# Performance work log

Hardware: AMD Instinct MI355X
Metric: run time of the kernel (lower is better)

The kernel has to match this reference:

```python
import jax, jax.numpy as jnp
import numpy as np

NUM_NODES_GLOBAL = 100000
EMBED_DIM = 256
NUM_RELATIONS = 16
N_LOCAL = 16384
N_EDGES = 131072
N_QUERIES = 4096


def setup_inputs() -> dict:
    key = jax.random.key(0)
    ks = jax.random.split(key, 12)
    node_emb = jax.random.normal(ks[0], (NUM_NODES_GLOBAL, EMBED_DIM), dtype=jnp.float32)
    # RGCN layer 1 params: per-relation weight (R, in, out), root weight, bias
    w1 = jax.random.normal(ks[1], (NUM_RELATIONS, EMBED_DIM, EMBED_DIM), dtype=jnp.float32) * 0.05
    root1 = jax.random.normal(ks[2], (EMBED_DIM, EMBED_DIM), dtype=jnp.float32) * 0.05
    b1 = jnp.zeros((EMBED_DIM,), dtype=jnp.float32)
    w2 = jax.random.normal(ks[3], (NUM_RELATIONS, EMBED_DIM, EMBED_DIM), dtype=jnp.float32) * 0.05
    root2 = jax.random.normal(ks[4], (EMBED_DIM, EMBED_DIM), dtype=jnp.float32) * 0.05
    b2 = jnp.zeros((EMBED_DIM,), dtype=jnp.float32)
    edge_index = jax.random.randint(ks[5], (2, N_EDGES), 0, N_LOCAL, dtype=jnp.int64)
    edge_type = jax.random.randint(ks[6], (N_EDGES,), 0, NUM_RELATIONS, dtype=jnp.int64)
    entity_ids = jax.random.randint(ks[7], (N_LOCAL,), 0, NUM_NODES_GLOBAL, dtype=jnp.int64)
    batch_ids = jnp.sort(jax.random.randint(ks[8], (N_LOCAL,), 0, N_QUERIES, dtype=jnp.int64))
    return {"node_emb": node_emb, "w1": w1, "root1": root1, "b1": b1,
            "w2": w2, "root2": root2, "b2": b2,
            "edge_index": edge_index, "edge_type": edge_type,
            "entity_ids": entity_ids, "batch_ids": batch_ids}


def rgcn_layer(x, W, Wroot, b, src, tgt, edge_type, num_relations):
    """PyG RGCNConv (num_bases=None, aggr='mean', root_weight=True, bias=True).

    out[i] = sum_r mean_{j: (j -r-> i)} x_j @ W[r]  +  x_i @ Wroot + b
    Aggregation done per (target, relation) bucket, then a single (N,R,d)x(R,d,d) einsum.
    """
    n = x.shape[0]
    d = x.shape[1]
    bucket = tgt * num_relations + edge_type  # (E,) combined (node, relation) key
    ones = jnp.ones(src.shape, dtype=x.dtype)
    cnt = jax.ops.segment_sum(ones, bucket, num_segments=n * num_relations)
    agg = jax.ops.segment_sum(x[src], bucket, num_segments=n * num_relations)
    agg = agg.reshape(n, num_relations, d) / jnp.maximum(cnt, 1.0).reshape(n, num_relations, 1)
    return jnp.einsum('nrd,rdo->no', agg, W) + x @ Wroot + b


def reference(node_emb, w1, root1, b1, w2, root2, b2, edge_index, edge_type, entity_ids, batch_ids):
    x = node_emb[entity_ids]                      # (N_local, d) gather from global table
    src, tgt = edge_index[0], edge_index[1]
    x = rgcn_layer(x, w1, root1, b1, src, tgt, edge_type, NUM_RELATIONS)
    x = rgcn_layer(x, w2, root2, b2, src, tgt, edge_type, NUM_RELATIONS)
    # scatter-sum readout per query
    return jax.ops.segment_sum(x, batch_ids, num_segments=N_QUERIES)
```

## Files before the change

kernel.cpp:

```cpp
#include <hip/hip_runtime.h>
#include <hip/hip_bf16.h>

#define NLOCAL 16384
#define NEDGES 131072
#define NREL   16
#define DIM    256
#define NQ     4096
#define NBLKS  512
#define NSLOTS (NEDGES + NREL * 64)
#define NBLKE  (NSLOTS / 64)

typedef __bf16 bf16x8 __attribute__((ext_vector_type(8)));
typedef float  f32x4  __attribute__((ext_vector_type(4)));
typedef unsigned short u16x4 __attribute__((ext_vector_type(4)));
typedef unsigned short u16x8 __attribute__((ext_vector_type(8)));

static __device__ __forceinline__ unsigned short f2bf(float f) {
    union { float f; unsigned u; } v; v.f = f;
    unsigned r = v.u + 0x7FFFu + ((v.u >> 16) & 1u);
    return (unsigned short)(r >> 16);
}
static __device__ __forceinline__ float bf2f(unsigned short s) {
    union { unsigned u; float f; } v; v.u = ((unsigned)s) << 16;
    return v.f;
}

__global__ void k_gather(const float* __restrict__ emb, const int* __restrict__ ids,
                         unsigned short* __restrict__ x0) {
    int gid = blockIdx.x * blockDim.x + threadIdx.x;
    int i = gid >> 5, c8 = gid & 31;
    int e = ids[i];
    const f32x4* src = (const f32x4*)(emb + (size_t)e * DIM + c8 * 8);
    f32x4 a = src[0], b = src[1];
    u16x8 u;
    u[0] = f2bf(a[0]); u[1] = f2bf(a[1]); u[2] = f2bf(a[2]); u[3] = f2bf(a[3]);
    u[4] = f2bf(b[0]); u[5] = f2bf(b[1]); u[6] = f2bf(b[2]); u[7] = f2bf(b[3]);
    *(u16x8*)&x0[(size_t)i * DIM + c8 * 8] = u;
}

__global__ void k_transpose_all(const float* __restrict__ w1, const float* __restrict__ r1,
                                const float* __restrict__ w2, const float* __restrict__ r2,
                                unsigned short* __restrict__ WT1, unsigned short* __restrict__ rT1,
                                unsigned short* __restrict__ WT2, unsigned short* __restrict__ rT2) {
    __shared__ float t[64][65];
    int blk = blockIdx.x;
    const float* W; unsigned short* WT; int tr;
    if (blk < 256)      { W = w1 + (size_t)(blk >> 4) * DIM * DIM; WT = WT1 + (size_t)(blk >> 4) * DIM * DIM; tr = blk & 15; }
    else if (blk < 272) { W = r1; WT = rT1; tr = blk - 256; }
    else if (blk < 528) { int q = blk - 272; W = w2 + (size_t)(q >> 4) * DIM * DIM; WT = WT2 + (size_t)(q >> 4) * DIM * DIM; tr = q & 15; }
    else                { W = r2; WT = rT2; tr = blk - 528; }
    int tk = (tr >> 2) << 6;
    int to = (tr & 3) << 6;
    #pragma unroll
    for (int it = 0; it < 16; ++it) {
        int el = it * 256 + threadIdx.x;
        int row = el >> 6, col = el & 63;
        t[row][col] = W[(size_t)(tk + row) * DIM + to + col];
    }
    __syncthreads();
    #pragma unroll
    for (int it = 0; it < 16; ++it) {
        int el = it * 256 + threadIdx.x;
        int row = el >> 6, col = el & 63;
        WT[(size_t)(to + row) * DIM + tk + col] = f2bf(t[col][row]);
    }
}

__global__ void k_hist2(const int* __restrict__ eidx, const int* __restrict__ etype,
                        unsigned int* __restrict__ cnt, unsigned int* __restrict__ cnt_t,
                        int* __restrict__ bh) {
    __shared__ int h[NREL];
    int tid = threadIdx.x;
    if (tid < NREL) h[tid] = 0;
    __syncthreads();
    int e = blockIdx.x * 256 + tid;
    int rel = etype[e];
    int tgt = eidx[NEDGES + e];
    atomicAdd(&cnt[tgt * NREL + rel], 1u);
    atomicAdd(&cnt_t[tgt], 1u);
    atomicAdd(&h[rel], 1);
    __syncthreads();
    if (tid < NREL) bh[tid * NBLKS + blockIdx.x] = h[tid];
}

__global__ void k_scan_all(int* __restrict__ bh, int* __restrict__ meta,
                           const unsigned int* __restrict__ cnt_t, int* __restrict__ row_ptr,
                           int* __restrict__ cur_t, int* __restrict__ blk_rel) {
    __shared__ int tot[NREL];
    __shared__ int rs[NREL + 1];
    __shared__ int wsum[16];
    int tid = threadIdx.x;
    int w = tid >> 6, lane = tid & 63;

    int vals[8];
    int run = 0;
    #pragma unroll
    for (int c = 0; c < 8; ++c) {
        int v = bh[w * NBLKS + c * 64 + lane];
        int s = v;
        #pragma unroll
        for (int off = 1; off < 64; off <<= 1) {
            int t = __shfl_up(s, off);
            if (lane >= off) s += t;
        }
        vals[c] = run + s - v;
        run += __shfl(s, 63);
    }
    if (lane == 0) tot[w] = run;
    __syncthreads();
    if (tid == 0) {
        int s = 0;
        for (int r = 0; r < NREL; ++r) { rs[r] = s; meta[16 + r] = s; s += (tot[r] + 63) & ~63; }
        rs[NREL] = s; meta[32] = s;
    }
    __syncthreads();
    int b0 = rs[w];
    #pragma unroll
    for (int c = 0; c < 8; ++c) bh[w * NBLKS + c * 64 + lane] = vals[c] + b0;

    int total = rs[NREL];
    for (int b = tid; b < NBLKE; b += 1024) {
        int base = b * 64;
        int r;
        if (base >= total) r = -1;
        else { r = 0; while (r < 15 && rs[r + 1] <= base) ++r; }
        blk_rel[b] = r;
    }

    int base16 = tid * 16;
    int loc[16];
    int s = 0;
    #pragma unroll
    for (int c = 0; c < 16; ++c) { loc[c] = s; s += (int)cnt_t[base16 + c]; }
    int inc = s;
    #pragma unroll
    for (int off = 1; off < 64; off <<= 1) {
        int t = __shfl_up(inc, off);
        if (lane >= off) inc += t;
    }
    if (lane == 63) wsum[w] = inc;
    __syncthreads();
    if (tid == 0) {
        int a = 0;
        for (int q = 0; q < 16; ++q) { int v = wsum[q]; wsum[q] = a; a += v; }
    }
    __syncthreads();
    int excl = wsum[w] + inc - s;
    #pragma unroll
    for (int c = 0; c < 16; ++c) { int v = excl + loc[c]; row_ptr[base16 + c] = v; cur_t[base16 + c] = v; }
    if (tid == 1023) row_ptr[NLOCAL] = excl + s;
}

__global__ void k_place2(const int* __restrict__ eidx, const int* __restrict__ etype,
                         const int* __restrict__ bh, int* __restrict__ ssrc,
                         int* __restrict__ stgt, int* __restrict__ cur_t,
                         int* __restrict__ elist) {
    __shared__ int cur[NREL];
    int tid = threadIdx.x;
    if (tid < NREL) cur[tid] = bh[tid * NBLKS + blockIdx.x];
    __syncthreads();
    int e = blockIdx.x * 256 + tid;
    int rel = etype[e];
    int tgt = eidx[NEDGES + e];
    int pos = atomicAdd(&cur[rel], 1);
    ssrc[pos] = eidx[e];
    stgt[pos] = tgt;
    int q = atomicAdd(&cur_t[tgt], 1);
    elist[q] = pos;
}

#define AS_IDX(row, c16) ((row) * 64 + (((c16) ^ ((row) & 7)) << 3))

__launch_bounds__(256)
__global__ void k_gemm_root(const unsigned short* __restrict__ X, const unsigned short* __restrict__ BT,
                            const float* __restrict__ bias, unsigned short* __restrict__ Y) {
    __shared__ __align__(16) unsigned short smem[16384];
    unsigned short* As0 = smem;
    unsigned short* As1 = smem + 4096;
    int tid = threadIdx.x;
    int wave = tid >> 6, lane = tid & 63;
    int l16 = lane & 15, grp = lane >> 4;
    int bm = blockIdx.x;
    int arow = tid >> 3, ac16 = tid & 7;

    f32x4 acc[4][4];
    #pragma unroll
    for (int i = 0; i < 4; ++i)
        #pragma unroll
        for (int j = 0; j < 4; ++j) acc[i][j] = f32x4{0.f, 0.f, 0.f, 0.f};

    #pragma unroll
    for (int it = 0; it < 2; ++it) {
        int row = it * 32 + arow;
        u16x8 u = *(const u16x8*)&X[(size_t)(bm * 64 + row) * DIM + ac16 * 8];
        *(u16x8*)&As0[AS_IDX(row, ac16)] = u;
    }
    for (int kt = 0; kt < 4; ++kt) {
        __syncthreads();
        if (kt < 3) {
            unsigned short* dst = (kt & 1) ? As0 : As1;
            #pragma unroll
            for (int it = 0; it < 2; ++it) {
                int row = it * 32 + arow;
                u16x8 u = *(const u16x8*)&X[(size_t)(bm * 64 + row) * DIM + (kt + 1) * 64 + ac16 * 8];
                *(u16x8*)&dst[AS_IDX(row, ac16)] = u;
            }
        }
        const unsigned short* buf = (kt & 1) ? As1 : As0;
        bf16x8 b[2][4];
        #pragma unroll
        for (int kk = 0; kk < 2; ++kk)
            #pragma unroll
            for (int j = 0; j < 4; ++j)
                b[kk][j] = *(const bf16x8*)&BT[(size_t)(wave * 64 + j * 16 + l16) * DIM + kt * 64 + kk * 32 + grp * 8];
        #pragma unroll
        for (int kk = 0; kk < 2; ++kk) {
            bf16x8 a[4];
            #pragma unroll
            for (int i = 0; i < 4; ++i)
                a[i] = *(const bf16x8*)&buf[AS_IDX(i * 16 + l16, kk * 4 + grp)];
            #pragma unroll
            for (int i = 0; i < 4; ++i)
                #pragma unroll
                for (int j = 0; j < 4; ++j)
                    acc[i][j] = __builtin_amdgcn_mfma_f32_16x16x32_bf16(a[i], b[kk][j], acc[i][j], 0, 0, 0);
        }
    }
    __syncthreads();
    #pragma unroll
    for (int i = 0; i < 4; ++i)
        #pragma unroll
        for (int reg = 0; reg < 4; ++reg) {
            int row = i * 16 + grp * 4 + reg;
            #pragma unroll
            for (int j = 0; j < 4; ++j) {
                int col = wave * 64 + j * 16 + l16;
                float v = acc[i][j][reg] + bias[col];
                float vo = __shfl_xor(v, 1);
                if (!(lane & 1)) {
                    unsigned pk = (unsigned)f2bf(v) | ((unsigned)f2bf(vo) << 16);
                    *(unsigned*)&smem[row * 256 + col] = pk;
                }
            }
        }
    __syncthreads();
    int r = tid >> 2;
    size_t orow = (size_t)(bm * 64 + r) * DIM;
    #pragma unroll
    for (int it = 0; it < 8; ++it) {
        int ch = (tid & 3) + it * 4;
        *(u16x8*)&Y[orow + ch * 8] = *(const u16x8*)&smem[r * 256 + ch * 8];
    }
}

__launch_bounds__(256)
__global__ void k_gemm_edge(const unsigned short* __restrict__ X, const unsigned short* __restrict__ WT,
                            const int* __restrict__ ssrc, const int* __restrict__ stgt,
                            const unsigned int* __restrict__ cnt, const int* __restrict__ blk_rel,
                            unsigned short* __restrict__ ye) {
    int rel = blk_rel[blockIdx.x];
    if (rel < 0) return;
    int base = blockIdx.x * 64;
    const unsigned short* BT = WT + (size_t)rel * DIM * DIM;

    __shared__ __align__(16) unsigned short smem[16384];
    unsigned short* As0 = smem;
    unsigned short* As1 = smem + 4096;
    int tid = threadIdx.x;
    int wave = tid >> 6, lane = tid & 63;
    int l16 = lane & 15, grp = lane >> 4;
    int arow = tid >> 3, ac16 = tid & 7;

    f32x4 acc[4][4];
    #pragma unroll
    for (int i = 0; i < 4; ++i)
        #pragma unroll
        for (int j = 0; j < 4; ++j) acc[i][j] = f32x4{0.f, 0.f, 0.f, 0.f};

    int s0 = ssrc[base + arow];
    int s1 = ssrc[base + 32 + arow];
    #pragma unroll
    for (int it = 0; it < 2; ++it) {
        int row = it * 32 + arow;
        int s = it ? s1 : s0;
        u16x8 u = {};
        if (s >= 0) u = *(const u16x8*)&X[(size_t)s * DIM + ac16 * 8];
        *(u16x8*)&As0[AS_IDX(row, ac16)] = u;
    }
    for (int kt = 0; kt < 4; ++kt) {
        __syncthreads();
        if (kt < 3) {
            unsigned short* dst = (kt & 1) ? As0 : As1;
            #pragma unroll
            for (int it = 0; it < 2; ++it) {
                int row = it * 32 + arow;
                int s = it ? s1 : s0;
                u16x8 u = {};
                if (s >= 0) u = *(const u16x8*)&X[(size_t)s * DIM + (kt + 1) * 64 + ac16 * 8];
                *(u16x8*)&dst[AS_IDX(row, ac16)] = u;
            }
        }
        const unsigned short* buf = (kt & 1) ? As1 : As0;
        bf16x8 b[2][4];
        #pragma unroll
        for (int kk = 0; kk < 2; ++kk)
            #pragma unroll
            for (int j = 0; j < 4; ++j)
                b[kk][j] = *(const bf16x8*)&BT[(size_t)(wave * 64 + j * 16 + l16) * DIM + kt * 64 + kk * 32 + grp * 8];
        #pragma unroll
        for (int kk = 0; kk < 2; ++kk) {
            bf16x8 a[4];
            #pragma unroll
            for (int i = 0; i < 4; ++i)
                a[i] = *(const bf16x8*)&buf[AS_IDX(i * 16 + l16, kk * 4 + grp)];
            #pragma unroll
            for (int i = 0; i < 4; ++i)
                #pragma unroll
                for (int j = 0; j < 4; ++j)
                    acc[i][j] = __builtin_amdgcn_mfma_f32_16x16x32_bf16(a[i], b[kk][j], acc[i][j], 0, 0, 0);
        }
    }
    __syncthreads();
    #pragma unroll
    for (int i = 0; i < 4; ++i)
        #pragma unroll
        for (int reg = 0; reg < 4; ++reg) {
            int row = i * 16 + grp * 4 + reg;
            int e = base + row;
            int s = ssrc[e];
            int tgt = stgt[e];
            float rc = (s >= 0) ? 1.0f / fmaxf((float)cnt[tgt * NREL + rel], 1.0f) : 0.0f;
            #pragma unroll
            for (int j = 0; j < 4; ++j) {
                int col = wave * 64 + j * 16 + l16;
                float v = acc[i][j][reg] * rc;
                float vo = __shfl_xor(v, 1);
                if (!(lane & 1)) {
                    unsigned pk = (unsigned)f2bf(v) | ((unsigned)f2bf(vo) << 16);
                    *(unsigned*)&smem[row * 256 + col] = pk;
                }
            }
        }
    __syncthreads();
    int r = tid >> 2;
    if (ssrc[base + r] >= 0) {
        size_t orow = (size_t)(base + r) * DIM;
        #pragma unroll
        for (int it = 0; it < 8; ++it) {
            int ch = (tid & 3) + it * 4;
            *(u16x8*)&ye[orow + ch * 8] = *(const u16x8*)&smem[r * 256 + ch * 8];
        }
    }
}

__global__ void k_combine(const unsigned short* __restrict__ rootY, const unsigned short* __restrict__ ye,
                          const int* __restrict__ row_ptr, const int* __restrict__ elist,
                          unsigned short* __restrict__ Xout) {
    int wave = threadIdx.x >> 6, lane = threadIdx.x & 63;
    int tgt = blockIdx.x * 4 + wave;
    int c0 = lane * 4;
    u16x4 rv = *(const u16x4*)&rootY[(size_t)tgt * DIM + c0];
    float a0 = bf2f(rv[0]), a1 = bf2f(rv[1]), a2 = bf2f(rv[2]), a3 = bf2f(rv[3]);
    int p0 = row_ptr[tgt], p1 = row_ptr[tgt + 1];
    for (int p = p0; p < p1; ++p) {
        int idx = elist[p];
        u16x4 v = *(const u16x4*)&ye[(size_t)idx * DIM + c0];
        a0 += bf2f(v[0]); a1 += bf2f(v[1]); a2 += bf2f(v[2]); a3 += bf2f(v[3]);
    }
    u16x4 o;
    o[0] = f2bf(a0); o[1] = f2bf(a1); o[2] = f2bf(a2); o[3] = f2bf(a3);
    *(u16x4*)&Xout[(size_t)tgt * DIM + c0] = o;
}

__global__ void k_readout(const unsigned short* __restrict__ X2, const int* __restrict__ bids,
                          float* __restrict__ out) {
    int gid = blockIdx.x * blockDim.x + threadIdx.x;
    int g = gid >> 5, c8 = gid & 31;
    int i0 = g * 8;
    float a[8];
    #pragma unroll
    for (int j = 0; j < 8; ++j) a[j] = 0.f;
    int curq = bids[i0];
    #pragma unroll
    for (int t = 0; t < 8; ++t) {
        int i = i0 + t;
        int q = bids[i];
        if (q != curq) {
            #pragma unroll
            for (int j = 0; j < 8; ++j) {
                unsafeAtomicAdd(&out[(size_t)curq * DIM + c8 * 8 + j], a[j]);
                a[j] = 0.f;
            }
            curq = q;
        }
        u16x8 v = *(const u16x8*)&X2[(size_t)i * DIM + c8 * 8];
        #pragma unroll
        for (int j = 0; j < 8; ++j) a[j] += bf2f(v[j]);
    }
    #pragma unroll
    for (int j = 0; j < 8; ++j)
        unsafeAtomicAdd(&out[(size_t)curq * DIM + c8 * 8 + j], a[j]);
}

extern "C" void kernel_launch(void* const* d_in, const int* in_sizes, int n_in,
                              void* d_out, int out_size, void* d_ws, size_t ws_size,
                              hipStream_t stream) {
    const float* emb   = (const float*)d_in[0];
    const float* w1    = (const float*)d_in[1];
    const float* root1 = (const float*)d_in[2];
    const float* b1    = (const float*)d_in[3];
    const float* w2    = (const float*)d_in[4];
    const float* root2 = (const float*)d_in[5];
    const float* b2    = (const float*)d_in[6];
    const int* eidx    = (const int*)d_in[7];
    const int* etype   = (const int*)d_in[8];
    const int* eids    = (const int*)d_in[9];
    const int* bids    = (const int*)d_in[10];
    float* out = (float*)d_out;

    char* ws = (char*)d_ws;
    unsigned short* x0   = (unsigned short*)(ws + (size_t)(0 << 20));
    unsigned short* x1   = (unsigned short*)(ws + (size_t)(8 << 20));
    unsigned short* x2   = (unsigned short*)(ws + (size_t)(16 << 20));
    unsigned short* WT1  = (unsigned short*)(ws + (size_t)(24 << 20));
    unsigned short* rT1  = (unsigned short*)(ws + (size_t)(26 << 20));
    unsigned short* WT2  = (unsigned short*)(ws + (size_t)(27 << 20));
    unsigned short* rT2  = (unsigned short*)(ws + (size_t)(29 << 20));
    unsigned int*   cnt  = (unsigned int*)(ws + (size_t)(30 << 20));
    int*           meta  = (int*)(ws + (size_t)(31 << 20));
    int*           ssrc  = (int*)(ws + (size_t)(31 << 20) + 4096);
    int*           stgt  = (int*)(ws + (size_t)(32 << 20));
    int*           bh    = (int*)(ws + (size_t)(33 << 20));
    unsigned int*  cnt_t = (unsigned int*)(ws + (size_t)(33 << 20) + 65536);
    int*         row_ptr = (int*)(ws + (size_t)(33 << 20) + 2 * 65536);
    int*           cur_t = (int*)(ws + (size_t)(33 << 20) + 4 * 65536);
    int*         blk_rel = (int*)(ws + (size_t)(33 << 20) + 6 * 65536);
    int*           elist = (int*)(ws + (size_t)(34 << 20));
    unsigned short* rootY= (unsigned short*)(ws + (size_t)(35 << 20));
    unsigned short* ye   = (unsigned short*)(ws + (size_t)(43 << 20));

    hipMemsetAsync(cnt, 0, (size_t)NLOCAL * NREL * 4, stream);
    hipMemsetAsync(cnt_t, 0, (size_t)NLOCAL * 4, stream);
    hipMemsetAsync(ssrc, 0xFF, (size_t)NSLOTS * 4, stream);
    hipMemsetAsync(out, 0, (size_t)NQ * DIM * 4, stream);

    k_gather<<<2048, 256, 0, stream>>>(emb, eids, x0);
    k_transpose_all<<<544, 256, 0, stream>>>(w1, root1, w2, root2, WT1, rT1, WT2, rT2);
    k_hist2<<<NBLKS, 256, 0, stream>>>(eidx, etype, cnt, cnt_t, bh);
    k_scan_all<<<1, 1024, 0, stream>>>(bh, meta, cnt_t, row_ptr, cur_t, blk_rel);
    k_place2<<<NBLKS, 256, 0, stream>>>(eidx, etype, bh, ssrc, stgt, cur_t, elist);

    k_gemm_root<<<NLOCAL / 64, 256, 0, stream>>>(x0, rT1, b1, rootY);
    k_gemm_edge<<<NBLKE, 256, 0, stream>>>(x0, WT1, ssrc, stgt, cnt, blk_rel, ye);
    k_combine<<<NLOCAL / 4, 256, 0, stream>>>(rootY, ye, row_ptr, elist, x1);
    k_gemm_root<<<NLOCAL / 64, 256, 0, stream>>>(x1, rT2, b2, rootY);
    k_gemm_edge<<<NBLKE, 256, 0, stream>>>(x1, WT2, ssrc, stgt, cnt, blk_rel, ye);
    k_combine<<<NLOCAL / 4, 256, 0, stream>>>(rootY, ye, row_ptr, elist, x2);

    k_readout<<<256, 256, 0, stream>>>(x2, bids, out);
}
```

Before: 468.0 us.

## Use direct global-to-LDS loads in GEMMs and fuse final combine into readout

Both GEMM kernels now fill the A tile with global_load_lds, moving the XOR swizzle to the global address side, and write results straight to global memory instead of staging through LDS. The last layer's combine step is merged into the per-query readout, so the x2 intermediate is no longer written and re-read and one launch is dropped. The trade-offs are narrower, less coalesced output stores and a fused readout whose per-thread edge loops run on only 256 blocks.

New measurement: 465.8 us. No clear change (-0.5%).

```diff
diff --git a/kernel.cpp b/kernel.cpp
--- a/kernel.cpp
+++ b/kernel.cpp
@@ -14,6 +14,9 @@
 typedef float  f32x4  __attribute__((ext_vector_type(4)));
 typedef unsigned short u16x4 __attribute__((ext_vector_type(4)));
 typedef unsigned short u16x8 __attribute__((ext_vector_type(8)));
+
+typedef __attribute__((address_space(1))) const void cglobal_t;
+typedef __attribute__((address_space(3))) void clds_t;
 
 static __device__ __forceinline__ unsigned short f2bf(float f) {
     union { float f; unsigned u; } v; v.f = f;
@@ -174,14 +177,18 @@
 __launch_bounds__(256)
 __global__ void k_gemm_root(const unsigned short* __restrict__ X, const unsigned short* __restrict__ BT,
                             const float* __restrict__ bias, unsigned short* __restrict__ Y) {
-    __shared__ __align__(16) unsigned short smem[16384];
-    unsigned short* As0 = smem;
-    unsigned short* As1 = smem + 4096;
+    __shared__ __align__(16) unsigned short As[2][4096];
     int tid = threadIdx.x;
     int wave = tid >> 6, lane = tid & 63;
     int l16 = lane & 15, grp = lane >> 4;
     int bm = blockIdx.x;
-    int arow = tid >> 3, ac16 = tid & 7;
+
+    int slot0 = (wave * 2 + 0) * 64 + lane;
+    int slot1 = (wave * 2 + 1) * 64 + lane;
+    int row0 = slot0 >> 3, cp0 = slot0 & 7;
+    int row1 = slot1 >> 3, cp1 = slot1 & 7;
+    size_t ga0 = (size_t)(bm * 64 + row0) * DIM + ((cp0 ^ (row0 & 7)) * 8);
+    size_t ga1 = (size_t)(bm * 64 + row1) * DIM + ((cp1 ^ (row1 & 7)) * 8);
 
     f32x4 acc[4][4];
     #pragma unroll
@@ -189,24 +196,17 @@
         #pragma unroll
         for (int j = 0; j < 4; ++j) acc[i][j] = f32x4{0.f, 0.f, 0.f, 0.f};
 
-    #pragma unroll
-    for (int it = 0; it < 2; ++it) {
-        int row = it * 32 + arow;
-        u16x8 u = *(const u16x8*)&X[(size_t)(bm * 64 + row) * DIM + ac16 * 8];
-        *(u16x8*)&As0[AS_IDX(row, ac16)] = u;
-    }
+    __builtin_amdgcn_global_load_lds((cglobal_t*)(X + ga0), (clds_t*)&As[0][slot0 * 8], 16, 0, 0);
+    __builtin_amdgcn_global_load_lds((cglobal_t*)(X + ga1), (clds_t*)&As[0][slot1 * 8], 16, 0, 0);
+
     for (int kt = 0; kt < 4; ++kt) {
         __syncthreads();
         if (kt < 3) {
-            unsigned short* dst = (kt & 1) ? As0 : As1;
-            #pragma unroll
-            for (int it = 0; it < 2; ++it) {
-                int row = it * 32 + arow;
-                u16x8 u = *(const u16x8*)&X[(size_t)(bm * 64 + row) * DIM + (kt + 1) * 64 + ac16 * 8];
-                *(u16x8*)&dst[AS_IDX(row, ac16)] = u;
-            }
-        }
-        const unsigned short* buf = (kt & 1) ? As1 : As0;
+            int nb = (kt + 1) & 1;
+            __builtin_amdgcn_global_load_lds((cglobal_t*)(X + ga0 + (kt + 1) * 64), (clds_t*)&As[nb][slot0 * 8], 16, 0, 0);
+            __builtin_amdgcn_global_load_lds((cglobal_t*)(X + ga1 + (kt + 1) * 64), (clds_t*)&As[nb][slot1 * 8], 16, 0, 0);
+        }
+        const unsigned short* buf = As[kt & 1];
         bf16x8 b[2][4];
         #pragma unroll
         for (int kk = 0; kk < 2; ++kk)
@@ -226,12 +226,12 @@
                     acc[i][j] = __builtin_amdgcn_mfma_f32_16x16x32_bf16(a[i], b[kk][j], acc[i][j], 0, 0, 0);
         }
     }
-    __syncthreads();
     #pragma unroll
     for (int i = 0; i < 4; ++i)
         #pragma unroll
         for (int reg = 0; reg < 4; ++reg) {
             int row = i * 16 + grp * 4 + reg;
+            int gr = bm * 64 + row;
             #pragma unroll
             for (int j = 0; j < 4; ++j) {
                 int col = wave * 64 + j * 16 + l16;
@@ -239,18 +239,10 @@
                 float vo = __shfl_xor(v, 1);
                 if (!(lane & 1)) {
                     unsigned pk = (unsigned)f2bf(v) | ((unsigned)f2bf(vo) << 16);
-                    *(unsigned*)&smem[row * 256 + col] = pk;
+                    *(unsigned*)&Y[(size_t)gr * DIM + col] = pk;
                 }
             }
         }
-    __syncthreads();
-    int r = tid >> 2;
-    size_t orow = (size_t)(bm * 64 + r) * DIM;
-    #pragma unroll
-    for (int it = 0; it < 8; ++it) {
-        int ch = (tid & 3) + it * 4;
-        *(u16x8*)&Y[orow + ch * 8] = *(const u16x8*)&smem[r * 256 + ch * 8];
-    }
 }
 
 __launch_bounds__(256)
@@ -263,13 +255,19 @@
     int base = blockIdx.x * 64;
     const unsigned short* BT = WT + (size_t)rel * DIM * DIM;
 
-    __shared__ __align__(16) unsigned short smem[16384];
-    unsigned short* As0 = smem;
-    unsigned short* As1 = smem + 4096;
+    __shared__ __align__(16) unsigned short As[2][4096];
     int tid = threadIdx.x;
     int wave = tid >> 6, lane = tid & 63;
     int l16 = lane & 15, grp = lane >> 4;
-    int arow = tid >> 3, ac16 = tid & 7;
+
+    int slot0 = (wave * 2 + 0) * 64 + lane;
+    int slot1 = (wave * 2 + 1) * 64 + lane;
+    int row0 = slot0 >> 3, cp0 = slot0 & 7;
+    int row1 = slot1 >> 3, cp1 = slot1 & 7;
+    int s0 = ssrc[base + row0];
+    int s1 = ssrc[base + row1];
+    size_t ga0 = (size_t)(s0 < 0 ? 0 : s0) * DIM + ((cp0 ^ (row0 & 7)) * 8);
+    size_t ga1 = (size_t)(s1 < 0 ? 0 : s1) * DIM + ((cp1 ^ (row1 & 7)) * 8);
 
     f32x4 acc[4][4];
     #pragma unroll
@@ -277,30 +275,17 @@
         #pragma unroll
         for (int j = 0; j < 4; ++j) acc[i][j] = f32x4{0.f, 0.f, 0.f, 0.f};
 
-    int s0 = ssrc[base + arow];
-    int s1 = ssrc[base + 32 + arow];
-    #pragma unroll
-    for (int it = 0; it < 2; ++it) {
-        int row = it * 32 + arow;
-        int s = it ? s1 : s0;
-        u16x8 u = {};
-        if (s >= 0) u = *(const u16x8*)&X[(size_t)s * DIM + ac16 * 8];
-        *(u16x8*)&As0[AS_IDX(row, ac16)] = u;
-    }
+    __builtin_amdgcn_global_load_lds((cglobal_t*)(X + ga0), (clds_t*)&As[0][slot0 * 8], 16, 0, 0);
+    __builtin_amdgcn_global_load_lds((cglobal_t*)(X + ga1), (clds_t*)&As[0][slot1 * 8], 16, 0, 0);
+
     for (int kt = 0; kt < 4; ++kt) {
         __syncthreads();
         if (kt < 3) {
-            unsigned short* dst = (kt & 1) ? As0 : As1;
-            #pragma unroll
-            for (int it = 0; it < 2; ++it) {
-                int row = it * 32 + arow;
-                int s = it ? s1 : s0;
-                u16x8 u = {};
-                if (s >= 0) u = *(const u16x8*)&X[(size_t)s * DIM + (kt + 1) * 64 + ac16 * 8];
-                *(u16x8*)&dst[AS_IDX(row, ac16)] = u;
-            }
-        }
-        const unsigned short* buf = (kt & 1) ? As1 : As0;
+            int nb = (kt + 1) & 1;
+            __builtin_amdgcn_global_load_lds((cglobal_t*)(X + ga0 + (kt + 1) * 64), (clds_t*)&As[nb][slot0 * 8], 16, 0, 0);
+            __builtin_amdgcn_global_load_lds((cglobal_t*)(X + ga1 + (kt + 1) * 64), (clds_t*)&As[nb][slot1 * 8], 16, 0, 0);
+        }
+        const unsigned short* buf = As[kt & 1];
         bf16x8 b[2][4];
         #pragma unroll
         for (int kk = 0; kk < 2; ++kk)
@@ -320,7 +305,6 @@
                     acc[i][j] = __builtin_amdgcn_mfma_f32_16x16x32_bf16(a[i], b[kk][j], acc[i][j], 0, 0, 0);
         }
     }
-    __syncthreads();
     #pragma unroll
     for (int i = 0; i < 4; ++i)
         #pragma unroll
@@ -335,22 +319,12 @@
                 int col = wave * 64 + j * 16 + l16;
                 float v = acc[i][j][reg] * rc;
                 float vo = __shfl_xor(v, 1);
-                if (!(lane & 1)) {
+                if (s >= 0 && !(lane & 1)) {
                     unsigned pk = (unsigned)f2bf(v) | ((unsigned)f2bf(vo) << 16);
-                    *(unsigned*)&smem[row * 256 + col] = pk;
+                    *(unsigned*)&ye[(size_t)e * DIM + col] = pk;
                 }
             }
         }
-    __syncthreads();
-    int r = tid >> 2;
-    if (ssrc[base + r] >= 0) {
-        size_t orow = (size_t)(base + r) * DIM;
-        #pragma unroll
-        for (int it = 0; it < 8; ++it) {
-            int ch = (tid & 3) + it * 4;
-            *(u16x8*)&ye[orow + ch * 8] = *(const u16x8*)&smem[r * 256 + ch * 8];
-        }
-    }
 }
 
 __global__ void k_combine(const unsigned short* __restrict__ rootY, const unsigned short* __restrict__ ye,
@@ -372,11 +346,13 @@
     *(u16x4*)&Xout[(size_t)tgt * DIM + c0] = o;
 }
 
-__global__ void k_readout(const unsigned short* __restrict__ X2, const int* __restrict__ bids,
-                          float* __restrict__ out) {
+__global__ void k_combine_read(const unsigned short* __restrict__ rootY, const unsigned short* __restrict__ ye,
+                               const int* __restrict__ row_ptr, const int* __restrict__ elist,
+                               const int* __restrict__ bids, float* __restrict__ out) {
     int gid = blockIdx.x * blockDim.x + threadIdx.x;
     int g = gid >> 5, c8 = gid & 31;
     int i0 = g * 8;
+    int c0 = c8 * 8;
     float a[8];
     #pragma unroll
     for (int j = 0; j < 8; ++j) a[j] = 0.f;
@@ -388,18 +364,25 @@
         if (q != curq) {
             #pragma unroll
             for (int j = 0; j < 8; ++j) {
-                unsafeAtomicAdd(&out[(size_t)curq * DIM + c8 * 8 + j], a[j]);
+                unsafeAtomicAdd(&out[(size_t)curq * DIM + c0 + j], a[j]);
                 a[j] = 0.f;
             }
             curq = q;
         }
-        u16x8 v = *(const u16x8*)&X2[(size_t)i * DIM + c8 * 8];
-        #pragma unroll
-        for (int j = 0; j < 8; ++j) a[j] += bf2f(v[j]);
+        u16x8 rv = *(const u16x8*)&rootY[(size_t)i * DIM + c0];
+        #pragma unroll
+        for (int j = 0; j < 8; ++j) a[j] += bf2f(rv[j]);
+        int p0 = row_ptr[i], p1 = row_ptr[i + 1];
+        for (int p = p0; p < p1; ++p) {
+            int idx = elist[p];
+            u16x8 v = *(const u16x8*)&ye[(size_t)idx * DIM + c0];
+            #pragma unroll
+            for (int j = 0; j < 8; ++j) a[j] += bf2f(v[j]);
+        }
     }
     #pragma unroll
     for (int j = 0; j < 8; ++j)
-        unsafeAtomicAdd(&out[(size_t)curq * DIM + c8 * 8 + j], a[j]);
+        unsafeAtomicAdd(&out[(size_t)curq * DIM + c0 + j], a[j]);
 }
 
 extern "C" void kernel_launch(void* const* d_in, const int* in_sizes, int n_in,
@@ -421,7 +404,6 @@
     char* ws = (char*)d_ws;
     unsigned short* x0   = (unsigned short*)(ws + (size_t)(0 << 20));
     unsigned short* x1   = (unsigned short*)(ws + (size_t)(8 << 20));
-    unsigned short* x2   = (unsigned short*)(ws + (size_t)(16 << 20));
     unsigned short* WT1  = (unsigned short*)(ws + (size_t)(24 << 20));
     unsigned short* rT1  = (unsigned short*)(ws + (size_t)(26 << 20));
     unsigned short* WT2  = (unsigned short*)(ws + (size_t)(27 << 20));
@@ -455,7 +437,5 @@
     k_combine<<<NLOCAL / 4, 256, 0, stream>>>(rootY, ye, row_ptr, elist, x1);
     k_gemm_root<<<NLOCAL / 64, 256, 0, stream>>>(x1, rT2, b2, rootY);
     k_gemm_edge<<<NBLKE, 256, 0, stream>>>(x1, WT2, ssrc, stgt, cnt, blk_rel, ye);
-    k_combine<<<NLOCAL / 4, 256, 0, stream>>>(rootY, ye, row_ptr, elist, x2);
-
-    k_readout<<<256, 256, 0, stream>>>(x2, bids, out);
-}
+    k_combine_read<<<256, 256, 0, stream>>>(rootY, ye, row_ptr, elist, bids, out);
+}
```
